# Performance work log

Measured on AMD Instinct MI355X. Metric: run time of the kernel, lower is better.

Reference implementation:

```python
import jax, jax.numpy as jnp
import numpy as np

DIM = 64
NUM_HEADS = 2
SR = 2


def _conv(x, w, stride):
    # x: [B,C,H,W], w: [O,I,kh,kw], no bias (qkv_bias=False)
    return jax.lax.conv_general_dilated(
        x, w, window_strides=(stride, stride), padding='VALID',
        dimension_numbers=('NCHW', 'OIHW', 'NCHW'))


def setup_inputs() -> dict:
    key = jax.random.key(0)
    kx, kq, kk, kv, kp = jax.random.split(key, 5)
    x = jax.random.normal(kx, (16, DIM, 64, 64), dtype=jnp.float32)
    s = 0.05
    wq = jax.random.normal(kq, (DIM, DIM, 1, 1), dtype=jnp.float32) * s
    wk = jax.random.normal(kk, (DIM, DIM, SR, SR), dtype=jnp.float32) * s
    wv = jax.random.normal(kv, (DIM, DIM, SR, SR), dtype=jnp.float32) * s
    wproj = jax.random.normal(kp, (DIM, DIM, 1, 1), dtype=jnp.float32) * s
    return {'x': x, 'wq': wq, 'wk': wk, 'wv': wv, 'wproj': wproj}


def reference(x, wq, wk, wv, wproj):
    B, C, H, W = x.shape
    h = NUM_HEADS
    hd = C // h
    scale = hd ** (-0.5)
    # Q: 1x1 conv, keeps spatial size; K/V: sr x sr conv with stride sr
    q = _conv(x, wq, 1).reshape(B, h, hd, -1)        # [B,h,hd,N]
    k = _conv(x, wk, SR).reshape(B, h, hd, -1)       # [B,h,hd,Nkv]
    v = _conv(x, wv, SR).reshape(B, h, hd, -1)       # [B,h,hd,Nkv]
    # attn = q^T @ k * scale -> [B,h,N,Nkv]
    attn = jnp.einsum('bhdn,bhdm->bhnm', q, k) * scale
    attn = jax.nn.softmax(attn, axis=-1)
    # out = v @ attn^T -> [B,h,hd,N]
    out = jnp.einsum('bhdm,bhnm->bhdn', v, attn)
    out = out.reshape(B, C, H, W)
    return _conv(out, wproj, 1)
```

## Files before the change

kernel.cpp:

```cpp
#include <hip/hip_runtime.h>
#include <hip/hip_bf16.h>


#define B_ 16
#define C_ 64
#define N_ 4096
#define NKV_ 1024

typedef __bf16 bf16x8 __attribute__((ext_vector_type(8)));
typedef __bf16 bf16x4 __attribute__((ext_vector_type(4)));
typedef float f32x4 __attribute__((ext_vector_type(4)));

__global__ __launch_bounds__(256) void conv1x1_k(const float* __restrict__ X,
                                                 const float* __restrict__ W,
                                                 float* __restrict__ Y) {
    __shared__ float xs[64][132];
    __shared__ float ws[64][65];
    const int b = blockIdx.x;
    const int n0 = blockIdx.y * 128;
    const int t = threadIdx.x;

    for (int idx = t; idx < 64 * 64; idx += 256) ws[idx >> 6][idx & 63] = W[idx];
    const float* Xb = X + (size_t)b * C_ * N_ + n0;
    for (int idx = t; idx < 64 * 128; idx += 256) {
        int ci = idx >> 7, n = idx & 127;
        xs[ci][n] = Xb[ci * N_ + n];
    }
    __syncthreads();

    const int co0 = (t >> 4) * 4;
    const int nn0 = (t & 15) * 8;
    float acc[4][8];
#pragma unroll
    for (int k = 0; k < 4; ++k)
#pragma unroll
        for (int j = 0; j < 8; ++j) acc[k][j] = 0.f;

    for (int ci = 0; ci < 64; ++ci) {
        float w0 = ws[co0 + 0][ci], w1 = ws[co0 + 1][ci];
        float w2 = ws[co0 + 2][ci], w3 = ws[co0 + 3][ci];
        float4 xa = *(const float4*)&xs[ci][nn0];
        float4 xb = *(const float4*)&xs[ci][nn0 + 4];
        float xv[8] = {xa.x, xa.y, xa.z, xa.w, xb.x, xb.y, xb.z, xb.w};
#pragma unroll
        for (int j = 0; j < 8; ++j) {
            acc[0][j] = fmaf(w0, xv[j], acc[0][j]);
            acc[1][j] = fmaf(w1, xv[j], acc[1][j]);
            acc[2][j] = fmaf(w2, xv[j], acc[2][j]);
            acc[3][j] = fmaf(w3, xv[j], acc[3][j]);
        }
    }
    float* Yb = Y + (size_t)b * C_ * N_ + n0;
#pragma unroll
    for (int k = 0; k < 4; ++k) {
        float4 o0 = {acc[k][0], acc[k][1], acc[k][2], acc[k][3]};
        float4 o1 = {acc[k][4], acc[k][5], acc[k][6], acc[k][7]};
        *(float4*)&Yb[(co0 + k) * N_ + nn0] = o0;
        *(float4*)&Yb[(co0 + k) * N_ + nn0 + 4] = o1;
    }
}

__global__ __launch_bounds__(256) void qconv_k(const float* __restrict__ X,
                                               const float* __restrict__ W,
                                               __bf16* __restrict__ Qt) {
    __shared__ float xs[64][132];
    __shared__ float ws[64][65];
    const int b = blockIdx.x;
    const int n0 = blockIdx.y * 128;
    const int t = threadIdx.x;
    const float scale = 0.17677669529663687f;

    for (int idx = t; idx < 64 * 64; idx += 256) ws[idx >> 6][idx & 63] = W[idx];
    const float* Xb = X + (size_t)b * C_ * N_ + n0;
    for (int idx = t; idx < 64 * 128; idx += 256) {
        int ci = idx >> 7, n = idx & 127;
        xs[ci][n] = Xb[ci * N_ + n];
    }
    __syncthreads();

    const int co0 = (t >> 4) * 4;
    const int nn0 = (t & 15) * 8;
    float acc[4][8];
#pragma unroll
    for (int k = 0; k < 4; ++k)
#pragma unroll
        for (int j = 0; j < 8; ++j) acc[k][j] = 0.f;

    for (int ci = 0; ci < 64; ++ci) {
        float w0 = ws[co0 + 0][ci], w1 = ws[co0 + 1][ci];
        float w2 = ws[co0 + 2][ci], w3 = ws[co0 + 3][ci];
        float4 xa = *(const float4*)&xs[ci][nn0];
        float4 xb = *(const float4*)&xs[ci][nn0 + 4];
        float xv[8] = {xa.x, xa.y, xa.z, xa.w, xb.x, xb.y, xb.z, xb.w};
#pragma unroll
        for (int j = 0; j < 8; ++j) {
            acc[0][j] = fmaf(w0, xv[j], acc[0][j]);
            acc[1][j] = fmaf(w1, xv[j], acc[1][j]);
            acc[2][j] = fmaf(w2, xv[j], acc[2][j]);
            acc[3][j] = fmaf(w3, xv[j], acc[3][j]);
        }
    }
    const int h = co0 >> 5, d0 = co0 & 31;
    __bf16* Qb = Qt + ((size_t)(b * 2 + h) * N_) * 32;
#pragma unroll
    for (int j = 0; j < 8; ++j) {
        int n = n0 + nn0 + j;
        bf16x4 v = {(__bf16)(acc[0][j] * scale), (__bf16)(acc[1][j] * scale),
                    (__bf16)(acc[2][j] * scale), (__bf16)(acc[3][j] * scale)};
        *(bf16x4*)&Qb[(size_t)n * 32 + d0] = v;
    }
}

__global__ __launch_bounds__(256) void convkv_k(const float* __restrict__ X,
                                                const float* __restrict__ Wk,
                                                const float* __restrict__ Wv,
                                                __bf16* __restrict__ Kt,
                                                __bf16* __restrict__ Vh) {
    __shared__ float xs[64][64];
    __shared__ float wks[64][65];
    __shared__ float wvs[64][65];
    const int b = blockIdx.x;
    const int m0 = blockIdx.y * 64;
    const int i0 = m0 >> 5;
    const int t = threadIdx.x;
    const int co0 = (t >> 4) * 4;
    const int mm0 = (t & 15) * 4;

    float accK[4][4], accV[4][4];
#pragma unroll
    for (int k = 0; k < 4; ++k)
#pragma unroll
        for (int m = 0; m < 4; ++m) { accK[k][m] = 0.f; accV[k][m] = 0.f; }

    const float* Xb = X + (size_t)b * C_ * N_;

    for (int ch = 0; ch < 4; ++ch) {
        for (int idx = t; idx < 4096; idx += 256) {
            int co = idx >> 6, rl = idx & 63;
            wks[co][rl] = Wk[co * 256 + ch * 64 + rl];
            wvs[co][rl] = Wv[co * 256 + ch * 64 + rl];
        }
        for (int idx = t; idx < 4096; idx += 256) {
            int rl = idx >> 6, ml = idx & 63;
            int ci = ch * 16 + (rl >> 2);
            int di = (rl >> 1) & 1, dj = rl & 1;
            int i = i0 + (ml >> 5), j = ml & 31;
            xs[rl][ml] = Xb[ci * N_ + (2 * i + di) * 64 + (2 * j + dj)];
        }
        __syncthreads();
        for (int rl = 0; rl < 64; ++rl) {
            float4 xv4 = *(const float4*)&xs[rl][mm0];
            float xa[4] = {xv4.x, xv4.y, xv4.z, xv4.w};
#pragma unroll
            for (int k = 0; k < 4; ++k) {
                float wk = wks[co0 + k][rl];
                float wv = wvs[co0 + k][rl];
#pragma unroll
                for (int m = 0; m < 4; ++m) {
                    accK[k][m] = fmaf(wk, xa[m], accK[k][m]);
                    accV[k][m] = fmaf(wv, xa[m], accV[k][m]);
                }
            }
        }
        __syncthreads();
    }
    const int h = co0 >> 5, d0 = co0 & 31;
    __bf16* Kb = Kt + ((size_t)(b * 2 + h) * NKV_) * 32;
    __bf16* Vb = Vh + ((size_t)(b * 2 + h) * 32) * NKV_;
#pragma unroll
    for (int m = 0; m < 4; ++m) {
        int mg = m0 + mm0 + m;
        bf16x4 kv = {(__bf16)accK[0][m], (__bf16)accK[1][m],
                     (__bf16)accK[2][m], (__bf16)accK[3][m]};
        *(bf16x4*)&Kb[(size_t)mg * 32 + d0] = kv;
    }
#pragma unroll
    for (int k = 0; k < 4; ++k) {
        bf16x4 vv = {(__bf16)accV[k][0], (__bf16)accV[k][1],
                     (__bf16)accV[k][2], (__bf16)accV[k][3]};
        *(bf16x4*)&Vb[(size_t)(d0 + k) * NKV_ + m0 + mm0] = vv;
    }
}

__global__ __launch_bounds__(256) void attn_mfma(const __bf16* __restrict__ Qt,
                                                 const __bf16* __restrict__ Kt,
                                                 const __bf16* __restrict__ Vh,
                                                 float* __restrict__ O) {
    __shared__ __bf16 Pls[4][2][16][40];
    const int bh = blockIdx.x;
    const int w = threadIdx.x >> 6;
    const int l = threadIdx.x & 63;
    const int lr = l & 15;
    const int lg = l >> 4;
    const int nb = blockIdx.y * 128 + w * 32;

    const __bf16* Qb = Qt + (size_t)bh * N_ * 32;
    const __bf16* Kb = Kt + (size_t)bh * NKV_ * 32;
    const __bf16* Vb = Vh + (size_t)bh * 32 * NKV_;

    bf16x8 qf[2];
    qf[0] = *(const bf16x8*)&Qb[(size_t)(nb + lr) * 32 + 8 * lg];
    qf[1] = *(const bf16x8*)&Qb[(size_t)(nb + 16 + lr) * 32 + 8 * lg];

    f32x4 oacc[2][2];
#pragma unroll
    for (int t = 0; t < 2; ++t)
#pragma unroll
        for (int dh = 0; dh < 2; ++dh) oacc[t][dh] = (f32x4){0.f, 0.f, 0.f, 0.f};
    float lsum[2][4] = {{0.f, 0.f, 0.f, 0.f}, {0.f, 0.f, 0.f, 0.f}};

    for (int mb = 0; mb < NKV_; mb += 32) {
#pragma unroll
        for (int mt = 0; mt < 2; ++mt) {
            bf16x8 kf = *(const bf16x8*)&Kb[(size_t)(mb + mt * 16 + lr) * 32 + 8 * lg];
#pragma unroll
            for (int t = 0; t < 2; ++t) {
                f32x4 s = __builtin_amdgcn_mfma_f32_16x16x32_bf16(
                    qf[t], kf, (f32x4){0.f, 0.f, 0.f, 0.f}, 0, 0, 0);
#pragma unroll
                for (int r = 0; r < 4; ++r) {
                    float p = __expf(s[r]);
                    lsum[t][r] += p;
                    Pls[w][t][4 * lg + r][mt * 16 + lr] = (__bf16)p;
                }
            }
        }
#pragma unroll
        for (int t = 0; t < 2; ++t) {
            bf16x8 af = *(const bf16x8*)&Pls[w][t][lr][8 * lg];
#pragma unroll
            for (int dh = 0; dh < 2; ++dh) {
                bf16x8 vf = *(const bf16x8*)&Vb[(size_t)(dh * 16 + lr) * NKV_ + mb + 8 * lg];
                oacc[t][dh] = __builtin_amdgcn_mfma_f32_16x16x32_bf16(af, vf, oacc[t][dh], 0, 0, 0);
            }
        }
    }

#pragma unroll
    for (int off = 1; off < 16; off <<= 1)
#pragma unroll
        for (int t = 0; t < 2; ++t)
#pragma unroll
            for (int r = 0; r < 4; ++r)
                lsum[t][r] += __shfl_xor(lsum[t][r], off, 64);

    const int b = bh >> 1, h = bh & 1;
#pragma unroll
    for (int t = 0; t < 2; ++t) {
        float inv[4];
#pragma unroll
        for (int r = 0; r < 4; ++r) inv[r] = 1.0f / lsum[t][r];
#pragma unroll
        for (int dh = 0; dh < 2; ++dh) {
            float4 ov = {oacc[t][dh][0] * inv[0], oacc[t][dh][1] * inv[1],
                         oacc[t][dh][2] * inv[2], oacc[t][dh][3] * inv[3]};
            size_t c = (size_t)b * 64 + h * 32 + dh * 16 + lr;
            *(float4*)&O[c * N_ + nb + t * 16 + 4 * lg] = ov;
        }
    }
}

extern "C" void kernel_launch(void* const* d_in, const int* in_sizes, int n_in,
                              void* d_out, int out_size, void* d_ws, size_t ws_size,
                              hipStream_t stream) {
    const float* x     = (const float*)d_in[0];
    const float* wq    = (const float*)d_in[1];
    const float* wk    = (const float*)d_in[2];
    const float* wv    = (const float*)d_in[3];
    const float* wproj = (const float*)d_in[4];
    float* out = (float*)d_out;

    char* ws = (char*)d_ws;
    __bf16* Qt = (__bf16*)ws;
    __bf16* Kt = (__bf16*)(ws + 8388608);
    __bf16* Vh = (__bf16*)(ws + 8388608 + 2097152);
    float*  O  = (float*)(ws + 8388608 + 2097152 + 2097152);

    qconv_k <<<dim3(B_, N_ / 128), 256, 0, stream>>>(x, wq, Qt);
    convkv_k<<<dim3(B_, NKV_ / 64), 256, 0, stream>>>(x, wk, wv, Kt, Vh);
    attn_mfma<<<dim3(B_ * 2, N_ / 128), 256, 0, stream>>>(Qt, Kt, Vh, O);
    conv1x1_k<<<dim3(B_, N_ / 128), 256, 0, stream>>>(O, wproj, out);
}
```

Before: 179.4 us.

## Rework attention tiling, split K/V conv grid, and fold log2e into Q scale

The attention kernel now gives each wave 16 query rows instead of 32 and doubles the grid. It computes S transposed (K as the A operand) so each lane sums probabilities for a single query, and it uses exp2 with log2(e) folded into the Q scale. The K/V conv is split across a grid z dimension so each block computes only K or V, and thread-to-output mappings are swapped to make the Q and K stores more coalesced. The goal is more parallelism and occupancy and less exp and reduction work. The cost is that K and V are reloaded more often and the X gather in the KV conv is done twice.

```diff
diff --git a/kernel.cpp b/kernel.cpp
--- a/kernel.cpp
+++ b/kernel.cpp
@@ -68,7 +68,7 @@
     const int b = blockIdx.x;
     const int n0 = blockIdx.y * 128;
     const int t = threadIdx.x;
-    const float scale = 0.17677669529663687f;
+    const float scale = 0.25503487572f;
 
     for (int idx = t; idx < 64 * 64; idx += 256) ws[idx >> 6][idx & 63] = W[idx];
     const float* Xb = X + (size_t)b * C_ * N_ + n0;
@@ -78,8 +78,8 @@
     }
     __syncthreads();
 
-    const int co0 = (t >> 4) * 4;
-    const int nn0 = (t & 15) * 8;
+    const int co0 = (t & 15) * 4;
+    const int nn0 = (t >> 4) * 8;
     float acc[4][8];
 #pragma unroll
     for (int k = 0; k < 4; ++k)
@@ -101,13 +101,12 @@
         }
     }
     const int h = co0 >> 5, d0 = co0 & 31;
-    __bf16* Qb = Qt + ((size_t)(b * 2 + h) * N_) * 32;
+    __bf16* Qb = Qt + (size_t)(b * 2 + h) * N_ * 32;
 #pragma unroll
     for (int j = 0; j < 8; ++j) {
-        int n = n0 + nn0 + j;
         bf16x4 v = {(__bf16)(acc[0][j] * scale), (__bf16)(acc[1][j] * scale),
                     (__bf16)(acc[2][j] * scale), (__bf16)(acc[3][j] * scale)};
-        *(bf16x4*)&Qb[(size_t)n * 32 + d0] = v;
+        *(bf16x4*)&Qb[(size_t)(n0 + nn0 + j) * 32 + d0] = v;
     }
 }
 
@@ -117,28 +116,28 @@
                                                 __bf16* __restrict__ Kt,
                                                 __bf16* __restrict__ Vh) {
     __shared__ float xs[64][64];
-    __shared__ float wks[64][65];
-    __shared__ float wvs[64][65];
+    __shared__ float ws[64][65];
     const int b = blockIdx.x;
     const int m0 = blockIdx.y * 64;
+    const int kv = blockIdx.z;
     const int i0 = m0 >> 5;
     const int t = threadIdx.x;
-    const int co0 = (t >> 4) * 4;
-    const int mm0 = (t & 15) * 4;
-
-    float accK[4][4], accV[4][4];
+    const int co0 = kv ? (t >> 4) * 4 : (t & 15) * 4;
+    const int mm0 = kv ? (t & 15) * 4 : (t >> 4) * 4;
+    const float* Wsel = kv ? Wv : Wk;
+
+    float acc[4][4];
 #pragma unroll
     for (int k = 0; k < 4; ++k)
 #pragma unroll
-        for (int m = 0; m < 4; ++m) { accK[k][m] = 0.f; accV[k][m] = 0.f; }
+        for (int m = 0; m < 4; ++m) acc[k][m] = 0.f;
 
     const float* Xb = X + (size_t)b * C_ * N_;
 
     for (int ch = 0; ch < 4; ++ch) {
         for (int idx = t; idx < 4096; idx += 256) {
             int co = idx >> 6, rl = idx & 63;
-            wks[co][rl] = Wk[co * 256 + ch * 64 + rl];
-            wvs[co][rl] = Wv[co * 256 + ch * 64 + rl];
+            ws[co][rl] = Wsel[co * 256 + ch * 64 + rl];
         }
         for (int idx = t; idx < 4096; idx += 256) {
             int rl = idx >> 6, ml = idx & 63;
@@ -153,111 +152,91 @@
             float xa[4] = {xv4.x, xv4.y, xv4.z, xv4.w};
 #pragma unroll
             for (int k = 0; k < 4; ++k) {
-                float wk = wks[co0 + k][rl];
-                float wv = wvs[co0 + k][rl];
-#pragma unroll
-                for (int m = 0; m < 4; ++m) {
-                    accK[k][m] = fmaf(wk, xa[m], accK[k][m]);
-                    accV[k][m] = fmaf(wv, xa[m], accV[k][m]);
-                }
+                float wv = ws[co0 + k][rl];
+#pragma unroll
+                for (int m = 0; m < 4; ++m) acc[k][m] = fmaf(wv, xa[m], acc[k][m]);
             }
         }
         __syncthreads();
     }
     const int h = co0 >> 5, d0 = co0 & 31;
-    __bf16* Kb = Kt + ((size_t)(b * 2 + h) * NKV_) * 32;
-    __bf16* Vb = Vh + ((size_t)(b * 2 + h) * 32) * NKV_;
-#pragma unroll
-    for (int m = 0; m < 4; ++m) {
-        int mg = m0 + mm0 + m;
-        bf16x4 kv = {(__bf16)accK[0][m], (__bf16)accK[1][m],
-                     (__bf16)accK[2][m], (__bf16)accK[3][m]};
-        *(bf16x4*)&Kb[(size_t)mg * 32 + d0] = kv;
-    }
-#pragma unroll
-    for (int k = 0; k < 4; ++k) {
-        bf16x4 vv = {(__bf16)accV[k][0], (__bf16)accV[k][1],
-                     (__bf16)accV[k][2], (__bf16)accV[k][3]};
-        *(bf16x4*)&Vb[(size_t)(d0 + k) * NKV_ + m0 + mm0] = vv;
-    }
-}
-
-__global__ __launch_bounds__(256) void attn_mfma(const __bf16* __restrict__ Qt,
-                                                 const __bf16* __restrict__ Kt,
-                                                 const __bf16* __restrict__ Vh,
-                                                 float* __restrict__ O) {
-    __shared__ __bf16 Pls[4][2][16][40];
+    if (kv) {
+        __bf16* Vb = Vh + (size_t)(b * 2 + h) * 32 * NKV_;
+#pragma unroll
+        for (int k = 0; k < 4; ++k) {
+            bf16x4 vv = {(__bf16)acc[k][0], (__bf16)acc[k][1],
+                         (__bf16)acc[k][2], (__bf16)acc[k][3]};
+            *(bf16x4*)&Vb[(size_t)(d0 + k) * NKV_ + m0 + mm0] = vv;
+        }
+    } else {
+        __bf16* Kb = Kt + (size_t)(b * 2 + h) * NKV_ * 32;
+#pragma unroll
+        for (int mq = 0; mq < 4; ++mq) {
+            bf16x4 kvv = {(__bf16)acc[0][mq], (__bf16)acc[1][mq],
+                          (__bf16)acc[2][mq], (__bf16)acc[3][mq]};
+            *(bf16x4*)&Kb[(size_t)(m0 + mm0 + mq) * 32 + d0] = kvv;
+        }
+    }
+}
+
+__global__ __launch_bounds__(256, 8) void attn_mfma(const __bf16* __restrict__ Qt,
+                                                    const __bf16* __restrict__ Kt,
+                                                    const __bf16* __restrict__ Vh,
+                                                    float* __restrict__ O) {
+    __shared__ __attribute__((aligned(16))) __bf16 Pls[4][16][40];
     const int bh = blockIdx.x;
     const int w = threadIdx.x >> 6;
     const int l = threadIdx.x & 63;
-    const int lr = l & 15;
-    const int lg = l >> 4;
-    const int nb = blockIdx.y * 128 + w * 32;
+    const int lr = l & 15, lg = l >> 4;
+    const int nb = blockIdx.y * 64 + w * 16;
 
     const __bf16* Qb = Qt + (size_t)bh * N_ * 32;
     const __bf16* Kb = Kt + (size_t)bh * NKV_ * 32;
     const __bf16* Vb = Vh + (size_t)bh * 32 * NKV_;
 
-    bf16x8 qf[2];
-    qf[0] = *(const bf16x8*)&Qb[(size_t)(nb + lr) * 32 + 8 * lg];
-    qf[1] = *(const bf16x8*)&Qb[(size_t)(nb + 16 + lr) * 32 + 8 * lg];
-
-    f32x4 oacc[2][2];
-#pragma unroll
-    for (int t = 0; t < 2; ++t)
-#pragma unroll
-        for (int dh = 0; dh < 2; ++dh) oacc[t][dh] = (f32x4){0.f, 0.f, 0.f, 0.f};
-    float lsum[2][4] = {{0.f, 0.f, 0.f, 0.f}, {0.f, 0.f, 0.f, 0.f}};
+    const bf16x8 qf = *(const bf16x8*)&Qb[(size_t)(nb + lr) * 32 + 8 * lg];
+    const __bf16* Krow = Kb + (size_t)lr * 32 + 8 * lg;
+    const __bf16* V0 = Vb + (size_t)lr * NKV_ + 8 * lg;
+    const __bf16* V1 = Vb + (size_t)(16 + lr) * NKV_ + 8 * lg;
+
+    f32x4 oacc0 = {0.f, 0.f, 0.f, 0.f}, oacc1 = {0.f, 0.f, 0.f, 0.f};
+    float lsum = 0.f;
 
     for (int mb = 0; mb < NKV_; mb += 32) {
-#pragma unroll
-        for (int mt = 0; mt < 2; ++mt) {
-            bf16x8 kf = *(const bf16x8*)&Kb[(size_t)(mb + mt * 16 + lr) * 32 + 8 * lg];
-#pragma unroll
-            for (int t = 0; t < 2; ++t) {
-                f32x4 s = __builtin_amdgcn_mfma_f32_16x16x32_bf16(
-                    qf[t], kf, (f32x4){0.f, 0.f, 0.f, 0.f}, 0, 0, 0);
-#pragma unroll
-                for (int r = 0; r < 4; ++r) {
-                    float p = __expf(s[r]);
-                    lsum[t][r] += p;
-                    Pls[w][t][4 * lg + r][mt * 16 + lr] = (__bf16)p;
-                }
-            }
-        }
-#pragma unroll
-        for (int t = 0; t < 2; ++t) {
-            bf16x8 af = *(const bf16x8*)&Pls[w][t][lr][8 * lg];
-#pragma unroll
-            for (int dh = 0; dh < 2; ++dh) {
-                bf16x8 vf = *(const bf16x8*)&Vb[(size_t)(dh * 16 + lr) * NKV_ + mb + 8 * lg];
-                oacc[t][dh] = __builtin_amdgcn_mfma_f32_16x16x32_bf16(af, vf, oacc[t][dh], 0, 0, 0);
-            }
-        }
-    }
-
-#pragma unroll
-    for (int off = 1; off < 16; off <<= 1)
-#pragma unroll
-        for (int t = 0; t < 2; ++t)
-#pragma unroll
-            for (int r = 0; r < 4; ++r)
-                lsum[t][r] += __shfl_xor(lsum[t][r], off, 64);
+        bf16x8 kf0 = *(const bf16x8*)&Krow[(size_t)mb * 32];
+        bf16x8 kf1 = *(const bf16x8*)&Krow[(size_t)(mb + 16) * 32];
+        f32x4 s0 = __builtin_amdgcn_mfma_f32_16x16x32_bf16(kf0, qf, (f32x4){0.f,0.f,0.f,0.f}, 0, 0, 0);
+        f32x4 s1 = __builtin_amdgcn_mfma_f32_16x16x32_bf16(kf1, qf, (f32x4){0.f,0.f,0.f,0.f}, 0, 0, 0);
+        float p0[4], p1[4];
+#pragma unroll
+        for (int r = 0; r < 4; ++r) {
+            p0[r] = __builtin_amdgcn_exp2f(s0[r]);
+            p1[r] = __builtin_amdgcn_exp2f(s1[r]);
+        }
+        lsum += ((p0[0] + p0[1]) + (p0[2] + p0[3])) + ((p1[0] + p1[1]) + (p1[2] + p1[3]));
+        bf16x4 w0 = {(__bf16)p0[0], (__bf16)p0[1], (__bf16)p0[2], (__bf16)p0[3]};
+        bf16x4 w1 = {(__bf16)p1[0], (__bf16)p1[1], (__bf16)p1[2], (__bf16)p1[3]};
+        *(bf16x4*)&Pls[w][lr][4 * lg] = w0;
+        *(bf16x4*)&Pls[w][lr][16 + 4 * lg] = w1;
+        bf16x8 af = *(const bf16x8*)&Pls[w][lr][8 * lg];
+        bf16x8 vf0 = *(const bf16x8*)&V0[mb];
+        bf16x8 vf1 = *(const bf16x8*)&V1[mb];
+        oacc0 = __builtin_amdgcn_mfma_f32_16x16x32_bf16(af, vf0, oacc0, 0, 0, 0);
+        oacc1 = __builtin_amdgcn_mfma_f32_16x16x32_bf16(af, vf1, oacc1, 0, 0, 0);
+    }
+
+    lsum += __shfl_xor(lsum, 16, 64);
+    lsum += __shfl_xor(lsum, 32, 64);
+    float inv[4];
+#pragma unroll
+    for (int r = 0; r < 4; ++r) inv[r] = 1.0f / __shfl(lsum, 4 * lg + r, 64);
 
     const int b = bh >> 1, h = bh & 1;
-#pragma unroll
-    for (int t = 0; t < 2; ++t) {
-        float inv[4];
-#pragma unroll
-        for (int r = 0; r < 4; ++r) inv[r] = 1.0f / lsum[t][r];
-#pragma unroll
-        for (int dh = 0; dh < 2; ++dh) {
-            float4 ov = {oacc[t][dh][0] * inv[0], oacc[t][dh][1] * inv[1],
-                         oacc[t][dh][2] * inv[2], oacc[t][dh][3] * inv[3]};
-            size_t c = (size_t)b * 64 + h * 32 + dh * 16 + lr;
-            *(float4*)&O[c * N_ + nb + t * 16 + 4 * lg] = ov;
-        }
-    }
+    float4 o0 = {oacc0[0] * inv[0], oacc0[1] * inv[1], oacc0[2] * inv[2], oacc0[3] * inv[3]};
+    float4 o1 = {oacc1[0] * inv[0], oacc1[1] * inv[1], oacc1[2] * inv[2], oacc1[3] * inv[3]};
+    const size_t c0 = (size_t)b * 64 + h * 32 + lr;
+    *(float4*)&O[c0 * N_ + nb + 4 * lg] = o0;
+    *(float4*)&O[(c0 + 16) * N_ + nb + 4 * lg] = o1;
 }
 
 extern "C" void kernel_launch(void* const* d_in, const int* in_sizes, int n_in,
@@ -277,7 +256,7 @@
     float*  O  = (float*)(ws + 8388608 + 2097152 + 2097152);
 
     qconv_k <<<dim3(B_, N_ / 128), 256, 0, stream>>>(x, wq, Qt);
-    convkv_k<<<dim3(B_, NKV_ / 64), 256, 0, stream>>>(x, wk, wv, Kt, Vh);
-    attn_mfma<<<dim3(B_ * 2, N_ / 128), 256, 0, stream>>>(Qt, Kt, Vh, O);
+    convkv_k<<<dim3(B_, NKV_ / 64, 2), 256, 0, stream>>>(x, wk, wv, Kt, Vh);
+    attn_mfma<<<dim3(B_ * 2, N_ / 64), 256, 0, stream>>>(Qt, Kt, Vh, O);
     conv1x1_k<<<dim3(B_, N_ / 128), 256, 0, stream>>>(O, wproj, out);
 }
```

Result: slower. 217.6 us (+21.3%).
